# Kernel tuning notes

Measured on AMD Instinct MI355X. Metric: run time of the kernel, lower is better.

Reference implementation:

```python
import jax, jax.numpy as jnp
import numpy as np

D = 1024      # input_dim
H = 4096      # hidden_dim
E = 8         # expert_count
TOP_K = 2
N = 8192      # tokens
LN_EPS = 1e-5


def setup_inputs() -> dict:
    key = jax.random.key(0)
    ks = jax.random.split(key, 10)
    s_d = 1.0 / np.sqrt(D)
    s_h = 1.0 / np.sqrt(H)
    return {
        "x": jax.random.normal(ks[0], (N, D), dtype=jnp.float32),
        "ln_gamma": jnp.ones((D,), jnp.float32),
        "ln_beta": jnp.zeros((D,), jnp.float32),
        "conf_w": jax.random.uniform(ks[1], (D, 1), jnp.float32, -s_d, s_d),
        "conf_b": jnp.zeros((1,), jnp.float32),
        "router_w": jax.random.uniform(ks[2], (D, E), jnp.float32, -s_d, s_d),
        "router_b": jnp.zeros((E,), jnp.float32),
        "w1": jax.random.uniform(ks[3], (E, D, H), jnp.float32, -s_d, s_d),
        "b1": jax.random.uniform(ks[4], (E, H), jnp.float32, -s_d, s_d),
        "w2": jax.random.uniform(ks[5], (E, H, D), jnp.float32, -s_h, s_h),
        "b2": jax.random.uniform(ks[6], (E, D), jnp.float32, -s_h, s_h),
    }


def reference(x, ln_gamma, ln_beta, conf_w, conf_b, router_w, router_b, w1, b1, w2, b2):
    # LayerNorm (torch default eps=1e-5, affine)
    mu = jnp.mean(x, axis=-1, keepdims=True)
    var = jnp.mean(jnp.square(x - mu), axis=-1, keepdims=True)
    x_norm = (x - mu) * jax.lax.rsqrt(var + LN_EPS) * ln_gamma + ln_beta

    # layer-skip confidence head
    confidence = jax.nn.sigmoid(x_norm @ conf_w + conf_b)  # [N,1]

    # router: softmax -> top-k -> renormalize selected weights
    router_probs = jax.nn.softmax(x_norm @ router_w + router_b, axis=-1)  # [N,E]
    vals, indices = jax.lax.top_k(router_probs, TOP_K)                    # [N,K]
    vals = vals / jnp.sum(vals, axis=-1, keepdims=True)

    # scatter top-k weights into dense per-expert combine weights [N,E]
    combine_w = jnp.zeros((x.shape[0], E), x.dtype).at[
        jnp.arange(x.shape[0])[:, None], indices].add(vals)

    # dispatch/combine: loop over small fixed expert count (dense compute,
    # weighted by combine_w, mathematically identical to per-token dispatch)
    combined = jnp.zeros_like(x)
    for e in range(E):
        h = jax.nn.relu(x_norm @ w1[e] + b1[e])      # [N,H]
        combined = combined + combine_w[:, e:e + 1] * (h @ w2[e] + b2[e])

    output = x + combined
    return output, confidence, x
```

## Files before the change

### kernel.cpp

```cpp
#include <hip/hip_runtime.h>
#include <hip/hip_bf16.h>

#define N_TOK 8192
#define DIM   1024
#define HID   4096
#define NEXP  8
#define CSTR  64
#define RTMAX 136
#define HROWS 16896

using bf16x8 = __attribute__((ext_vector_type(8))) short;
using f32x4  = __attribute__((ext_vector_type(4))) float;

__device__ __forceinline__ void gload_lds16(const void* g, void* l) {
  __builtin_amdgcn_global_load_lds(
      (const __attribute__((address_space(1))) unsigned int*)g,
      (__attribute__((address_space(3))) unsigned int*)l, 16, 0, 0);
}

__device__ __forceinline__ float wredsum(float v) {
#pragma unroll
  for (int off = 32; off > 0; off >>= 1) v += __shfl_xor(v, off, 64);
  return v;
}

__device__ __forceinline__ unsigned short f2bf(float f) {
  __hip_bfloat16 h = __float2bfloat16(f);
  return *reinterpret_cast<unsigned short*>(&h);
}
__device__ __forceinline__ float bf2f(unsigned short u) {
  return __uint_as_float((unsigned)u << 16);
}

__global__ __launch_bounds__(256) void prep_kernel(
    const float* __restrict__ x, const float* __restrict__ gamma, const float* __restrict__ beta,
    const float* __restrict__ conf_w, const float* __restrict__ conf_b,
    const float* __restrict__ rw, const float* __restrict__ rb,
    __hip_bfloat16* __restrict__ xn, float* __restrict__ out,
    int* __restrict__ counts, int* __restrict__ lists, float* __restrict__ wts,
    int2* __restrict__ idx) {
  const int t = blockIdx.x * 4 + (threadIdx.x >> 6);
  const int lane = threadIdx.x & 63;
  const float* xr = x + (size_t)t * DIM;

  float4 xv[4];
#pragma unroll
  for (int q = 0; q < 4; q++) xv[q] = *(const float4*)(xr + q * 256 + lane * 4);

  float s = 0.f, s2 = 0.f;
#pragma unroll
  for (int q = 0; q < 4; q++) {
    s  += xv[q].x + xv[q].y + xv[q].z + xv[q].w;
    s2 += xv[q].x * xv[q].x + xv[q].y * xv[q].y + xv[q].z * xv[q].z + xv[q].w * xv[q].w;
  }
  s = wredsum(s); s2 = wredsum(s2);
  const float mu  = s * (1.f / DIM);
  const float inv = rsqrtf(s2 * (1.f / DIM) - mu * mu + 1e-5f);

  float p[9];
#pragma unroll
  for (int e = 0; e < 9; e++) p[e] = 0.f;

#pragma unroll
  for (int q = 0; q < 4; q++) {
    const int d0 = q * 256 + lane * 4;
    const float4 g4 = *(const float4*)(gamma + d0);
    const float4 b4 = *(const float4*)(beta + d0);
    float v0 = (xv[q].x - mu) * inv * g4.x + b4.x;
    float v1 = (xv[q].y - mu) * inv * g4.y + b4.y;
    float v2 = (xv[q].z - mu) * inv * g4.z + b4.z;
    float v3 = (xv[q].w - mu) * inv * g4.w + b4.w;

    ushort4 st; st.x = f2bf(v0); st.y = f2bf(v1); st.z = f2bf(v2); st.w = f2bf(v3);
    *(ushort4*)((unsigned short*)xn + (size_t)t * DIM + d0) = st;
    *(float4*)(out + (size_t)t * DIM + d0) = xv[q];
    *(float4*)(out + (size_t)N_TOK * DIM + N_TOK + (size_t)t * DIM + d0) = xv[q];

    const float vv[4] = {v0, v1, v2, v3};
#pragma unroll
    for (int j = 0; j < 4; j++) {
      const int d = d0 + j;
      const float v = vv[j];
      p[8] += v * conf_w[d];
      const float4 r0 = *(const float4*)(rw + d * 8);
      const float4 r1 = *(const float4*)(rw + d * 8 + 4);
      p[0] += v * r0.x; p[1] += v * r0.y; p[2] += v * r0.z; p[3] += v * r0.w;
      p[4] += v * r1.x; p[5] += v * r1.y; p[6] += v * r1.z; p[7] += v * r1.w;
    }
  }
#pragma unroll
  for (int e = 0; e < 9; e++) p[e] = wredsum(p[e]);

  if (lane == 0) {
    float L[8];
#pragma unroll
    for (int e = 0; e < 8; e++) L[e] = p[e] + rb[e];
    const float cl = p[8] + conf_b[0];
    out[(size_t)N_TOK * DIM + t] = 1.f / (1.f + expf(-cl));

    float mx = L[0];
#pragma unroll
    for (int e = 1; e < 8; e++) mx = fmaxf(mx, L[e]);
    float pe[8];
#pragma unroll
    for (int e = 0; e < 8; e++) pe[e] = expf(L[e] - mx);
    int i0 = 0; float v0 = pe[0];
#pragma unroll
    for (int e = 1; e < 8; e++) if (pe[e] > v0) { v0 = pe[e]; i0 = e; }
    int i1 = -1; float v1 = -1.f;
#pragma unroll
    for (int e = 0; e < 8; e++) if (e != i0 && pe[e] > v1) { v1 = pe[e]; i1 = e; }
    const float wsum = v0 + v1;
    const float w0 = v0 / wsum, w1 = v1 / wsum;
    int p0 = atomicAdd(&counts[i0 * CSTR], 1);
    lists[i0 * N_TOK + p0] = t; wts[i0 * N_TOK + p0] = w0;
    int p1 = atomicAdd(&counts[i1 * CSTR], 1);
    lists[i1 * N_TOK + p1] = t; wts[i1 * N_TOK + p1] = w1;
    idx[t] = make_int2((i0 << 13) | p0, (i1 << 13) | p1);
  }
}

__global__ void bases_kernel(const int* __restrict__ counts, int* __restrict__ bases,
                             int* __restrict__ meta) {
  if (threadIdx.x == 0) {
    int s = 0, r = 0;
#pragma unroll
    for (int e = 0; e < NEXP; e++) {
      bases[e] = s; meta[e] = r;
      const int c = counts[e * CSTR];
      s += c; r += (c + 127) >> 7;
    }
    meta[NEXP] = r;
  }
}

__global__ __launch_bounds__(256) void transpose_cast64(
    const float* __restrict__ src0, __hip_bfloat16* __restrict__ dst0, int R, int C) {
  __shared__ float tile[64][65];
  const size_t msz = (size_t)R * C;
  const float* src = src0 + blockIdx.z * msz;
  __hip_bfloat16* dst = dst0 + blockIdx.z * msz;
  const int c0 = blockIdx.x * 64, r0 = blockIdx.y * 64;
  const int tid = threadIdx.x;
  const int tx = tid & 15, ty = tid >> 4;
#pragma unroll
  for (int k = 0; k < 4; k++) {
    const int row = ty + k * 16;
    const float4 v = *(const float4*)(src + (size_t)(r0 + row) * C + c0 + tx * 4);
    tile[row][tx * 4 + 0] = v.x; tile[row][tx * 4 + 1] = v.y;
    tile[row][tx * 4 + 2] = v.z; tile[row][tx * 4 + 3] = v.w;
  }
  __syncthreads();
#pragma unroll
  for (int k = 0; k < 4; k++) {
    const int orow = ty + k * 16;
    ushort4 st;
    st.x = f2bf(tile[tx * 4 + 0][orow]);
    st.y = f2bf(tile[tx * 4 + 1][orow]);
    st.z = f2bf(tile[tx * 4 + 2][orow]);
    st.w = f2bf(tile[tx * 4 + 3][orow]);
    *(ushort4*)((unsigned short*)dst + (size_t)(c0 + orow) * R + r0 + tx * 4) = st;
  }
}


#define GEMM_CORE(NT)                                                                   \
  f32x4 acc[4][4] = {};                                                                 \
  stage(0, 0); stage(1, 24576);                                                         \
  for (int t = 0; t < (NT); ++t) {                                                      \
    const int pb = (t % 3) * 24576;                                                     \
    if (t + 1 < (NT)) { asm volatile("s_waitcnt vmcnt(3)" ::: "memory"); }              \
    else              { asm volatile("s_waitcnt vmcnt(0)" ::: "memory"); }              \
    __builtin_amdgcn_s_barrier();                                                       \
    if (t + 2 < (NT)) stage(t + 2, ((t + 2) % 3) * 24576);                              \
    const char* Ab = smem + pb + Abase;                                                 \
    const char* Bb = smem + pb + Bbase;                                                 \
    bf16x8 bfr[4];                                                                      \
    _Pragma("unroll")                                                                   \
    for (int n = 0; n < 4; n++) bfr[n] = *(const bf16x8*)(Bb + n * 1024);               \
    _Pragma("unroll")                                                                   \
    for (int qq = 0; qq < 2; qq++) {                                                    \
      bf16x8 af0 = *(const bf16x8*)(Ab + (qq * 2 + 0) * 1024);                          \
      bf16x8 af1 = *(const bf16x8*)(Ab + (qq * 2 + 1) * 1024);                          \
      asm volatile("s_waitcnt lgkmcnt(0)" ::: "memory");                                \
      __builtin_amdgcn_sched_barrier(0);                                                \
      __builtin_amdgcn_s_setprio(1);                                                    \
      _Pragma("unroll")                                                                 \
      for (int n = 0; n < 4; n++) {                                                     \
        acc[qq * 2 + 0][n] = __builtin_amdgcn_mfma_f32_16x16x32_bf16(af0, bfr[n], acc[qq * 2 + 0][n], 0, 0, 0); \
        acc[qq * 2 + 1][n] = __builtin_amdgcn_mfma_f32_16x16x32_bf16(af1, bfr[n], acc[qq * 2 + 1][n], 0, 0, 0); \
      }                                                                                 \
      __builtin_amdgcn_s_setprio(0);                                                    \
    }                                                                                   \
  }

#define DECODE_BLOCK(PPX)                                                     \
  int panel, rtg;                                                             \
  if ((PPX) > 0) {                                                            \
    const int x_ = (int)blockIdx.x & 7;                                       \
    const int q_ = (int)blockIdx.x >> 3;                                      \
    rtg = q_ / (PPX);                                                         \
    panel = x_ * (PPX) + (q_ - rtg * (PPX));                                  \
  } else {                                                                    \
    panel = (int)blockIdx.x / RTMAX;                                          \
    rtg = (int)blockIdx.x - panel * RTMAX;                                    \
  }                                                                           \
  if (rtg >= meta[NEXP]) return;                                              \
  int e = 0;                                                                  \
  _Pragma("unroll")                                                           \
  for (int k = 1; k < NEXP; k++) if (meta[k] <= rtg) e = k;                   \
  const int rt = rtg - meta[e];                                               \
  const int cnt = counts[e * CSTR];                                           \
  const int hbase = bases[e];

#define GEMM_COMMON()                                                         \
  __shared__ char smem[73728];                                                \
  const int tid = threadIdx.x;                                                \
  const int l = tid & 63;                                                     \
  const int w8 = tid >> 6;                                                    \
  const int wr = w8 >> 2;                                                     \
  const int wc = w8 & 3;                                                      \
  const int lr = l & 15;                                                      \
  const int pchunk = (l >> 4) ^ ((lr >> 1) & 3);                              \
  const int Abase = (wr * 64 + lr) * 64 + pchunk * 16;                        \
  const int Bbase = 8192 + (wc * 64 + lr) * 64 + pchunk * 16;                 \
  const int srow = tid >> 2;                      \
  const int lc = (tid & 3) ^ ((srow >> 1) & 3);

__global__ __launch_bounds__(512, 4) void gemm1_kernel(
    const __hip_bfloat16* __restrict__ xn, const __hip_bfloat16* __restrict__ w1t_b,
    const float* __restrict__ b1, const int* __restrict__ lists,
    const int* __restrict__ counts, const int* __restrict__ bases,
    const int* __restrict__ meta, __hip_bfloat16* __restrict__ hbuf, const int ppx) {
  DECODE_BLOCK(ppx)
  const int ct = panel;
  const int* list = lists + e * N_TOK;
  const __hip_bfloat16* w1t = w1t_b + (size_t)e * DIM * HID;
  GEMM_COMMON()

  const int apos = rt * 128 + srow;
  const int tok = list[apos < cnt ? apos : 0];
  const unsigned short* srcA0 = (const unsigned short*)xn + (size_t)tok * DIM + lc * 8;
  const unsigned short* srcB0 = (const unsigned short*)w1t + (size_t)(ct * 256 + srow) * DIM + lc * 8;
  const unsigned short* srcB1 = (const unsigned short*)w1t + (size_t)(ct * 256 + 128 + srow) * DIM + lc * 8;

  auto stage = [&](int tt, int lbase) {
    gload_lds16(srcA0 + tt * 32, smem + lbase + tid * 16);
    gload_lds16(srcB0 + tt * 32, smem + lbase + 8192 + tid * 16);
    gload_lds16(srcB1 + tt * 32, smem + lbase + 16384 + tid * 16);
  };

  GEMM_CORE(DIM / 32)

  __builtin_amdgcn_s_barrier();
#pragma unroll
  for (int h = 0; h < 2; h++) {
    if (wr == h) {
#pragma unroll
      for (int n = 0; n < 4; n++) {
        const int col = wc * 64 + n * 16 + lr;
        const float bv = b1[e * HID + ct * 256 + col];
#pragma unroll
        for (int m = 0; m < 4; m++) {
          f32x4 v = acc[m][n];
#pragma unroll
          for (int j = 0; j < 4; j++)
            ((unsigned short*)smem)[(m * 16 + (l >> 4) * 4 + j) * 256 + col] =
                f2bf(fmaxf(v[j] + bv, 0.f));
        }
      }
    }
    asm volatile("s_waitcnt lgkmcnt(0)" ::: "memory");
    __builtin_amdgcn_s_barrier();
    const int g = tid >> 5, u = tid & 31;
#pragma unroll
    for (int i = 0; i < 4; i++) {
      const int row = i * 16 + g;
      const int pos = rt * 128 + h * 64 + row;
      if (pos < cnt) {
        bf16x8 vv = *(const bf16x8*)((const unsigned short*)smem + row * 256 + u * 8);
        *(bf16x8*)((unsigned short*)hbuf + (size_t)(hbase + pos) * HID + ct * 256 + u * 8) = vv;
      }
    }
    __builtin_amdgcn_s_barrier();
  }
}

__global__ __launch_bounds__(512, 4) void gemm2_kernel(
    const __hip_bfloat16* __restrict__ hbuf, const __hip_bfloat16* __restrict__ w2t_b,
    const int* __restrict__ counts, const int* __restrict__ bases,
    const int* __restrict__ meta, __hip_bfloat16* __restrict__ ybuf,
    const int SK, const int ppx) {
  DECODE_BLOCK(ppx)
  const int ct = panel & 3;
  const int ksp = panel >> 2;
  const int kbase = ksp * (HID / SK);
  const __hip_bfloat16* w2t = w2t_b + (size_t)e * DIM * HID;
  GEMM_COMMON()

  const unsigned short* srcA0 = (const unsigned short*)hbuf +
      (size_t)(hbase + rt * 128 + srow) * HID + kbase + lc * 8;
  const unsigned short* srcB0 = (const unsigned short*)w2t +
      (size_t)(ct * 256 + srow) * HID + kbase + lc * 8;
  const unsigned short* srcB1 = (const unsigned short*)w2t +
      (size_t)(ct * 256 + 128 + srow) * HID + kbase + lc * 8;

  auto stage = [&](int tt, int lbase) {
    gload_lds16(srcA0 + tt * 32, smem + lbase + tid * 16);
    gload_lds16(srcB0 + tt * 32, smem + lbase + 8192 + tid * 16);
    gload_lds16(srcB1 + tt * 32, smem + lbase + 16384 + tid * 16);
  };

  const int nk = (HID / 32) / SK;
  GEMM_CORE(nk)

  __builtin_amdgcn_s_barrier();
#pragma unroll
  for (int h = 0; h < 2; h++) {
    if (wr == h) {
#pragma unroll
      for (int n = 0; n < 4; n++) {
        const int col = wc * 64 + n * 16 + lr;
#pragma unroll
        for (int m = 0; m < 4; m++) {
          f32x4 v = acc[m][n];
#pragma unroll
          for (int j = 0; j < 4; j++)
            ((unsigned short*)smem)[(m * 16 + (l >> 4) * 4 + j) * 256 + col] = f2bf(v[j]);
        }
      }
    }
    asm volatile("s_waitcnt lgkmcnt(0)" ::: "memory");
    __builtin_amdgcn_s_barrier();
    const int g = tid >> 5, u = tid & 31;
#pragma unroll
    for (int i = 0; i < 4; i++) {
      const int row = i * 16 + g;
      const int pos = rt * 128 + h * 64 + row;
      if (pos < cnt) {
        bf16x8 vv = *(const bf16x8*)((const unsigned short*)smem + row * 256 + u * 8);
        *(bf16x8*)((unsigned short*)ybuf +
                   ((size_t)ksp * HROWS + hbase + pos) * DIM + ct * 256 + u * 8) = vv;
      }
    }
    __builtin_amdgcn_s_barrier();
  }
}

__global__ __launch_bounds__(256) void combine_kernel(
    const __hip_bfloat16* __restrict__ ybuf, const float* __restrict__ b2,
    const int2* __restrict__ idx, const float* __restrict__ wv,
    const int* __restrict__ bases, float* __restrict__ out, const int SK) {
  const int t = blockIdx.x * 4 + (threadIdx.x >> 6);
  const int lane = threadIdx.x & 63;
  const int2 iv = idx[t];
  const int e0 = iv.x >> 13, p0 = iv.x & (N_TOK - 1);
  const int e1 = iv.y >> 13, p1 = iv.y & (N_TOK - 1);
  const float w0 = wv[iv.x], w1 = wv[iv.y];
  const int r0 = bases[e0] + p0;
  const int r1 = bases[e1] + p1;
#pragma unroll
  for (int q = 0; q < 4; q++) {
    const int d0 = q * 256 + lane * 4;
    float4 o = *(const float4*)(out + (size_t)t * DIM + d0);
    float y0x = 0.f, y0y = 0.f, y0z = 0.f, y0w = 0.f;
    float y1x = 0.f, y1y = 0.f, y1z = 0.f, y1w = 0.f;
    for (int s = 0; s < SK; s++) {
      const ushort4 a = *(const ushort4*)((const unsigned short*)ybuf +
                          ((size_t)s * HROWS + r0) * DIM + d0);
      const ushort4 b = *(const ushort4*)((const unsigned short*)ybuf +
                          ((size_t)s * HROWS + r1) * DIM + d0);
      y0x += bf2f(a.x); y0y += bf2f(a.y); y0z += bf2f(a.z); y0w += bf2f(a.w);
      y1x += bf2f(b.x); y1y += bf2f(b.y); y1z += bf2f(b.z); y1w += bf2f(b.w);
    }
    const float4 bb0 = *(const float4*)(b2 + e0 * DIM + d0);
    const float4 bb1 = *(const float4*)(b2 + e1 * DIM + d0);
    o.x += w0 * (y0x + bb0.x) + w1 * (y1x + bb1.x);
    o.y += w0 * (y0y + bb0.y) + w1 * (y1y + bb1.y);
    o.z += w0 * (y0z + bb0.z) + w1 * (y1z + bb1.z);
    o.w += w0 * (y0w + bb0.w) + w1 * (y1w + bb1.w);
    *(float4*)(out + (size_t)t * DIM + d0) = o;
  }
}

extern "C" void kernel_launch(void* const* d_in, const int* in_sizes, int n_in,
                              void* d_out, int out_size, void* d_ws, size_t ws_size,
                              hipStream_t stream) {
  (void)in_sizes; (void)n_in; (void)out_size;
  const float* x      = (const float*)d_in[0];
  const float* gamma  = (const float*)d_in[1];
  const float* beta   = (const float*)d_in[2];
  const float* conf_w = (const float*)d_in[3];
  const float* conf_b = (const float*)d_in[4];
  const float* rw     = (const float*)d_in[5];
  const float* rb     = (const float*)d_in[6];
  const float* w1     = (const float*)d_in[7];
  const float* b1     = (const float*)d_in[8];
  const float* w2     = (const float*)d_in[9];
  const float* b2     = (const float*)d_in[10];
  float* out = (float*)d_out;

  char* w = (char*)d_ws;
  auto alloc = [&](size_t bytes) { char* p = w; w += (bytes + 255) & ~255ULL; return p; };

  __hip_bfloat16* xn = (__hip_bfloat16*)alloc((size_t)N_TOK * DIM * 2);
  int*   lists  = (int*)alloc((size_t)NEXP * N_TOK * 4);
  float* wtsb   = (float*)alloc((size_t)NEXP * N_TOK * 4);
  int*   counts = (int*)alloc(NEXP * CSTR * 4);
  int*   bases  = (int*)alloc(256);
  int*   meta   = (int*)alloc(256);
  int2*  idx    = (int2*)alloc((size_t)N_TOK * 8);

  const size_t hbufA = (size_t)HROWS * HID * 2;
  const size_t wtA   = (size_t)NEXP * DIM * HID * 2;
  __hip_bfloat16* hbuf = (__hip_bfloat16*)alloc(hbufA);
  __hip_bfloat16* w1t  = (__hip_bfloat16*)alloc(wtA);
  __hip_bfloat16* w2t  = (__hip_bfloat16*)alloc(wtA);
  const size_t used = (size_t)(w - (char*)d_ws);
  const size_t ybuf1 = (size_t)HROWS * DIM * 2;

  int SK;
  __hip_bfloat16* ybuf;
  if (ws_size >= used + 4 * ybuf1 + 4096) {
    SK = 4; ybuf = (__hip_bfloat16*)alloc(4 * ybuf1);
  } else if (ws_size >= used + 2 * ybuf1 + 4096) {
    SK = 2; ybuf = (__hip_bfloat16*)alloc(2 * ybuf1);
  } else {
    SK = 1; ybuf = w1t;
  }
  const int g2panels = 4 * SK;
  const int g2ppx = (SK == 4) ? 2 : (SK == 2 ? 1 : 0);
  const int g2grid = g2ppx > 0 ? 8 * g2ppx * RTMAX : g2panels * RTMAX;

  hipMemsetAsync(counts, 0, NEXP * CSTR * 4, stream);
  prep_kernel<<<N_TOK / 4, 256, 0, stream>>>(x, gamma, beta, conf_w, conf_b, rw, rb,
                                             xn, out, counts, lists, wtsb, idx);
  bases_kernel<<<1, 64, 0, stream>>>(counts, bases, meta);
  transpose_cast64<<<dim3(HID / 64, DIM / 64, NEXP), 256, 0, stream>>>(w1, w1t, DIM, HID);
  transpose_cast64<<<dim3(DIM / 64, HID / 64, NEXP), 256, 0, stream>>>(w2, w2t, HID, DIM);
  gemm1_kernel<<<8 * 2 * RTMAX, 512, 0, stream>>>(xn, w1t, b1, lists, counts, bases, meta,
                                                  hbuf, 2);
  gemm2_kernel<<<g2grid, 512, 0, stream>>>(hbuf, w2t, counts, bases, meta, ybuf, SK, g2ppx);
  combine_kernel<<<N_TOK / 4, 256, 0, stream>>>(ybuf, b2, idx, wtsb, bases, out, SK);
}
```

Before: 510.0 us.

## Fuse weight transposes into prep kernel, widen epilogue, reorder MFMA loop, drop SK=4

Folds the two weight transpose-cast launches into the LayerNorm/router prep kernel as extra blocks, which cuts launches and lets transposes overlap with routing work. The GEMM inner loop now loads all A fragments up front and issues 16 MFMAs behind a single wait. The epilogue stages the whole 128-row tile through padded LDS in one pass instead of two halves. The four-way split-K option for gemm2 is removed, so SK is at most 2. That reduces the partial-sum traffic but gives gemm2 less parallelism.

```diff
diff --git a/kernel.cpp b/kernel.cpp
--- a/kernel.cpp
+++ b/kernel.cpp
@@ -8,6 +8,7 @@
 #define CSTR  64
 #define RTMAX 136
 #define HROWS 16896
+#define EPS   264
 
 using bf16x8 = __attribute__((ext_vector_type(8))) short;
 using f32x4  = __attribute__((ext_vector_type(4))) float;
@@ -32,14 +33,58 @@
   return __uint_as_float((unsigned)u << 16);
 }
 
-__global__ __launch_bounds__(256) void prep_kernel(
+__device__ __forceinline__ void transpose_body(
+    const float* __restrict__ src, __hip_bfloat16* __restrict__ dst,
+    int R, int C, int c0, int r0, float (*tile)[65]) {
+  const int tid = threadIdx.x;
+  const int tx = tid & 15, ty = tid >> 4;
+#pragma unroll
+  for (int k = 0; k < 4; k++) {
+    const int row = ty + k * 16;
+    const float4 v = *(const float4*)(src + (size_t)(r0 + row) * C + c0 + tx * 4);
+    tile[row][tx * 4 + 0] = v.x; tile[row][tx * 4 + 1] = v.y;
+    tile[row][tx * 4 + 2] = v.z; tile[row][tx * 4 + 3] = v.w;
+  }
+  __syncthreads();
+#pragma unroll
+  for (int k = 0; k < 4; k++) {
+    const int orow = ty + k * 16;
+    ushort4 st;
+    st.x = f2bf(tile[tx * 4 + 0][orow]);
+    st.y = f2bf(tile[tx * 4 + 1][orow]);
+    st.z = f2bf(tile[tx * 4 + 2][orow]);
+    st.w = f2bf(tile[tx * 4 + 3][orow]);
+    *(ushort4*)((unsigned short*)dst + (size_t)(c0 + orow) * R + r0 + tx * 4) = st;
+  }
+}
+
+__global__ __launch_bounds__(256) void setup_kernel(
     const float* __restrict__ x, const float* __restrict__ gamma, const float* __restrict__ beta,
     const float* __restrict__ conf_w, const float* __restrict__ conf_b,
     const float* __restrict__ rw, const float* __restrict__ rb,
+    const float* __restrict__ w1, const float* __restrict__ w2,
+    __hip_bfloat16* __restrict__ w1t, __hip_bfloat16* __restrict__ w2t,
     __hip_bfloat16* __restrict__ xn, float* __restrict__ out,
     int* __restrict__ counts, int* __restrict__ lists, float* __restrict__ wts,
     int2* __restrict__ idx) {
-  const int t = blockIdx.x * 4 + (threadIdx.x >> 6);
+  __shared__ float tile[64][65];
+  const int b = (int)blockIdx.x;
+  if (b < 8192) {
+    const int z = b >> 10, r = b & 1023;
+    const int cx = r & 63, ry = r >> 6;
+    transpose_body(w1 + (size_t)z * DIM * HID, w1t + (size_t)z * DIM * HID,
+                   DIM, HID, cx * 64, ry * 64, tile);
+    return;
+  }
+  if (b < 16384) {
+    const int bb = b - 8192;
+    const int z = bb >> 10, r = bb & 1023;
+    const int cx = r & 15, ry = r >> 4;
+    transpose_body(w2 + (size_t)z * HID * DIM, w2t + (size_t)z * HID * DIM,
+                   HID, DIM, cx * 64, ry * 64, tile);
+    return;
+  }
+  const int t = (b - 16384) * 4 + ((int)threadIdx.x >> 6);
   const int lane = threadIdx.x & 63;
   const float* xr = x + (size_t)t * DIM;
 
@@ -111,11 +156,11 @@
 #pragma unroll
     for (int e = 0; e < 8; e++) if (e != i0 && pe[e] > v1) { v1 = pe[e]; i1 = e; }
     const float wsum = v0 + v1;
-    const float w0 = v0 / wsum, w1 = v1 / wsum;
+    const float w0 = v0 / wsum, w1v = v1 / wsum;
     int p0 = atomicAdd(&counts[i0 * CSTR], 1);
     lists[i0 * N_TOK + p0] = t; wts[i0 * N_TOK + p0] = w0;
     int p1 = atomicAdd(&counts[i1 * CSTR], 1);
-    lists[i1 * N_TOK + p1] = t; wts[i1 * N_TOK + p1] = w1;
+    lists[i1 * N_TOK + p1] = t; wts[i1 * N_TOK + p1] = w1v;
     idx[t] = make_int2((i0 << 13) | p0, (i1 << 13) | p1);
   }
 }
@@ -131,35 +176,6 @@
       s += c; r += (c + 127) >> 7;
     }
     meta[NEXP] = r;
-  }
-}
-
-__global__ __launch_bounds__(256) void transpose_cast64(
-    const float* __restrict__ src0, __hip_bfloat16* __restrict__ dst0, int R, int C) {
-  __shared__ float tile[64][65];
-  const size_t msz = (size_t)R * C;
-  const float* src = src0 + blockIdx.z * msz;
-  __hip_bfloat16* dst = dst0 + blockIdx.z * msz;
-  const int c0 = blockIdx.x * 64, r0 = blockIdx.y * 64;
-  const int tid = threadIdx.x;
-  const int tx = tid & 15, ty = tid >> 4;
-#pragma unroll
-  for (int k = 0; k < 4; k++) {
-    const int row = ty + k * 16;
-    const float4 v = *(const float4*)(src + (size_t)(r0 + row) * C + c0 + tx * 4);
-    tile[row][tx * 4 + 0] = v.x; tile[row][tx * 4 + 1] = v.y;
-    tile[row][tx * 4 + 2] = v.z; tile[row][tx * 4 + 3] = v.w;
-  }
-  __syncthreads();
-#pragma unroll
-  for (int k = 0; k < 4; k++) {
-    const int orow = ty + k * 16;
-    ushort4 st;
-    st.x = f2bf(tile[tx * 4 + 0][orow]);
-    st.y = f2bf(tile[tx * 4 + 1][orow]);
-    st.z = f2bf(tile[tx * 4 + 2][orow]);
-    st.w = f2bf(tile[tx * 4 + 3][orow]);
-    *(ushort4*)((unsigned short*)dst + (size_t)(c0 + orow) * R + r0 + tx * 4) = st;
   }
 }
 
@@ -175,23 +191,20 @@
     if (t + 2 < (NT)) stage(t + 2, ((t + 2) % 3) * 24576);                              \
     const char* Ab = smem + pb + Abase;                                                 \
     const char* Bb = smem + pb + Bbase;                                                 \
-    bf16x8 bfr[4];                                                                      \
+    bf16x8 bfr[4], afr[4];                                                              \
     _Pragma("unroll")                                                                   \
     for (int n = 0; n < 4; n++) bfr[n] = *(const bf16x8*)(Bb + n * 1024);               \
     _Pragma("unroll")                                                                   \
-    for (int qq = 0; qq < 2; qq++) {                                                    \
-      bf16x8 af0 = *(const bf16x8*)(Ab + (qq * 2 + 0) * 1024);                          \
-      bf16x8 af1 = *(const bf16x8*)(Ab + (qq * 2 + 1) * 1024);                          \
-      asm volatile("s_waitcnt lgkmcnt(0)" ::: "memory");                                \
-      __builtin_amdgcn_sched_barrier(0);                                                \
-      __builtin_amdgcn_s_setprio(1);                                                    \
+    for (int m = 0; m < 4; m++) afr[m] = *(const bf16x8*)(Ab + m * 1024);               \
+    asm volatile("s_waitcnt lgkmcnt(0)" ::: "memory");                                  \
+    __builtin_amdgcn_sched_barrier(0);                                                  \
+    __builtin_amdgcn_s_setprio(1);                                                      \
+    _Pragma("unroll")                                                                   \
+    for (int m = 0; m < 4; m++)                                                         \
       _Pragma("unroll")                                                                 \
-      for (int n = 0; n < 4; n++) {                                                     \
-        acc[qq * 2 + 0][n] = __builtin_amdgcn_mfma_f32_16x16x32_bf16(af0, bfr[n], acc[qq * 2 + 0][n], 0, 0, 0); \
-        acc[qq * 2 + 1][n] = __builtin_amdgcn_mfma_f32_16x16x32_bf16(af1, bfr[n], acc[qq * 2 + 1][n], 0, 0, 0); \
-      }                                                                                 \
-      __builtin_amdgcn_s_setprio(0);                                                    \
-    }                                                                                   \
+      for (int n = 0; n < 4; n++)                                                       \
+        acc[m][n] = __builtin_amdgcn_mfma_f32_16x16x32_bf16(afr[m], bfr[n], acc[m][n], 0, 0, 0); \
+    __builtin_amdgcn_s_setprio(0);                                                      \
   }
 
 #define DECODE_BLOCK(PPX)                                                     \
@@ -227,6 +240,37 @@
   const int srow = tid >> 2;                      \
   const int lc = (tid & 3) ^ ((srow >> 1) & 3);
 
+#define EPILOGUE(EXPR, DSTROW)                                                \
+  __builtin_amdgcn_s_barrier();                                               \
+  {                                                                           \
+    unsigned short* ep = (unsigned short*)smem;                               \
+    _Pragma("unroll")                                                         \
+    for (int n = 0; n < 4; n++) {                                             \
+      const int col = wc * 64 + n * 16 + lr;                                  \
+      _Pragma("unroll")                                                       \
+      for (int m = 0; m < 4; m++) {                                           \
+        f32x4 v = acc[m][n];                                                  \
+        _Pragma("unroll")                                                     \
+        for (int j = 0; j < 4; j++) {                                         \
+          const int row = wr * 64 + m * 16 + (l >> 4) * 4 + j;                \
+          ep[row * EPS + col] = (EXPR);                                       \
+        }                                                                     \
+      }                                                                       \
+    }                                                                         \
+    asm volatile("s_waitcnt lgkmcnt(0)" ::: "memory");                        \
+    __builtin_amdgcn_s_barrier();                                             \
+    const int g = tid >> 5, u = tid & 31;                                     \
+    _Pragma("unroll")                                                         \
+    for (int i = 0; i < 8; i++) {                                             \
+      const int row = i * 16 + g;                                             \
+      const int pos = rt * 128 + row;                                         \
+      if (pos < cnt) {                                                        \
+        bf16x8 vv = *(const bf16x8*)(ep + row * EPS + u * 8);                 \
+        *(bf16x8*)(DSTROW + u * 8) = vv;                                      \
+      }                                                                       \
+    }                                                                         \
+  }
+
 __global__ __launch_bounds__(512, 4) void gemm1_kernel(
     const __hip_bfloat16* __restrict__ xn, const __hip_bfloat16* __restrict__ w1t_b,
     const float* __restrict__ b1, const int* __restrict__ lists,
@@ -252,38 +296,19 @@
 
   GEMM_CORE(DIM / 32)
 
-  __builtin_amdgcn_s_barrier();
-#pragma unroll
-  for (int h = 0; h < 2; h++) {
-    if (wr == h) {
-#pragma unroll
-      for (int n = 0; n < 4; n++) {
-        const int col = wc * 64 + n * 16 + lr;
-        const float bv = b1[e * HID + ct * 256 + col];
-#pragma unroll
-        for (int m = 0; m < 4; m++) {
-          f32x4 v = acc[m][n];
-#pragma unroll
-          for (int j = 0; j < 4; j++)
-            ((unsigned short*)smem)[(m * 16 + (l >> 4) * 4 + j) * 256 + col] =
-                f2bf(fmaxf(v[j] + bv, 0.f));
-        }
-      }
-    }
-    asm volatile("s_waitcnt lgkmcnt(0)" ::: "memory");
-    __builtin_amdgcn_s_barrier();
-    const int g = tid >> 5, u = tid & 31;
-#pragma unroll
-    for (int i = 0; i < 4; i++) {
-      const int row = i * 16 + g;
-      const int pos = rt * 128 + h * 64 + row;
-      if (pos < cnt) {
-        bf16x8 vv = *(const bf16x8*)((const unsigned short*)smem + row * 256 + u * 8);
-        *(bf16x8*)((unsigned short*)hbuf + (size_t)(hbase + pos) * HID + ct * 256 + u * 8) = vv;
-      }
-    }
-    __builtin_amdgcn_s_barrier();
-  }
+  const float bv[4] = {
+    b1[e * HID + ct * 256 + wc * 64 + 0 * 16 + lr],
+    b1[e * HID + ct * 256 + wc * 64 + 1 * 16 + lr],
+    b1[e * HID + ct * 256 + wc * 64 + 2 * 16 + lr],
+    b1[e * HID + ct * 256 + wc * 64 + 3 * 16 + lr]};
+#pragma unroll
+  for (int n = 0; n < 4; n++)
+#pragma unroll
+    for (int m = 0; m < 4; m++)
+#pragma unroll
+      for (int j = 0; j < 4; j++) acc[m][n][j] = fmaxf(acc[m][n][j] + bv[n], 0.f);
+  EPILOGUE(f2bf(v[j]),
+           (unsigned short*)hbuf + (size_t)(hbase + pos) * HID + ct * 256)
 }
 
 __global__ __launch_bounds__(512, 4) void gemm2_kernel(
@@ -314,37 +339,8 @@
   const int nk = (HID / 32) / SK;
   GEMM_CORE(nk)
 
-  __builtin_amdgcn_s_barrier();
-#pragma unroll
-  for (int h = 0; h < 2; h++) {
-    if (wr == h) {
-#pragma unroll
-      for (int n = 0; n < 4; n++) {
-        const int col = wc * 64 + n * 16 + lr;
-#pragma unroll
-        for (int m = 0; m < 4; m++) {
-          f32x4 v = acc[m][n];
-#pragma unroll
-          for (int j = 0; j < 4; j++)
-            ((unsigned short*)smem)[(m * 16 + (l >> 4) * 4 + j) * 256 + col] = f2bf(v[j]);
-        }
-      }
-    }
-    asm volatile("s_waitcnt lgkmcnt(0)" ::: "memory");
-    __builtin_amdgcn_s_barrier();
-    const int g = tid >> 5, u = tid & 31;
-#pragma unroll
-    for (int i = 0; i < 4; i++) {
-      const int row = i * 16 + g;
-      const int pos = rt * 128 + h * 64 + row;
-      if (pos < cnt) {
-        bf16x8 vv = *(const bf16x8*)((const unsigned short*)smem + row * 256 + u * 8);
-        *(bf16x8*)((unsigned short*)ybuf +
-                   ((size_t)ksp * HROWS + hbase + pos) * DIM + ct * 256 + u * 8) = vv;
-      }
-    }
-    __builtin_amdgcn_s_barrier();
-  }
+  EPILOGUE(f2bf(v[j]),
+           (unsigned short*)ybuf + ((size_t)ksp * HROWS + hbase + pos) * DIM + ct * 256)
 }
 
 __global__ __launch_bounds__(256) void combine_kernel(
@@ -421,23 +417,19 @@
 
   int SK;
   __hip_bfloat16* ybuf;
-  if (ws_size >= used + 4 * ybuf1 + 4096) {
-    SK = 4; ybuf = (__hip_bfloat16*)alloc(4 * ybuf1);
-  } else if (ws_size >= used + 2 * ybuf1 + 4096) {
+  if (ws_size >= used + 2 * ybuf1 + 4096) {
     SK = 2; ybuf = (__hip_bfloat16*)alloc(2 * ybuf1);
   } else {
     SK = 1; ybuf = w1t;
   }
-  const int g2panels = 4 * SK;
-  const int g2ppx = (SK == 4) ? 2 : (SK == 2 ? 1 : 0);
-  const int g2grid = g2ppx > 0 ? 8 * g2ppx * RTMAX : g2panels * RTMAX;
+  const int g2ppx = (SK == 2) ? 1 : 0;
+  const int g2grid = g2ppx > 0 ? 8 * g2ppx * RTMAX : 4 * RTMAX;
 
   hipMemsetAsync(counts, 0, NEXP * CSTR * 4, stream);
-  prep_kernel<<<N_TOK / 4, 256, 0, stream>>>(x, gamma, beta, conf_w, conf_b, rw, rb,
-                                             xn, out, counts, lists, wtsb, idx);
+  setup_kernel<<<16384 + N_TOK / 4, 256, 0, stream>>>(
+      x, gamma, beta, conf_w, conf_b, rw, rb, w1, w2, w1t, w2t,
+      xn, out, counts, lists, wtsb, idx);
   bases_kernel<<<1, 64, 0, stream>>>(counts, bases, meta);
-  transpose_cast64<<<dim3(HID / 64, DIM / 64, NEXP), 256, 0, stream>>>(w1, w1t, DIM, HID);
-  transpose_cast64<<<dim3(DIM / 64, HID / 64, NEXP), 256, 0, stream>>>(w2, w2t, HID, DIM);
   gemm1_kernel<<<8 * 2 * RTMAX, 512, 0, stream>>>(xn, w1t, b1, lists, counts, bases, meta,
                                                   hbuf, 2);
   gemm2_kernel<<<g2grid, 512, 0, stream>>>(hbuf, w2t, counts, bases, meta, ybuf, SK, g2ppx);
```

Measured after the change: 494.4 us. -3.1%, faster.
